# Performance work log

Hardware: AMD Instinct MI355X
Metric: run time of the kernel (lower is better)

## Reference

```python
import jax, jax.numpy as jnp
import numpy as np

B, T, C = 4, 2048, 1024
H_DIM = 1024
N_HEADS = 16
MAX_T = 2048


def setup_inputs() -> dict:
    key = jax.random.key(0)
    ks = jax.random.split(key, 9)
    s = 1.0 / np.sqrt(C)
    return {
        "x": jax.random.normal(ks[0], (B, T, C), dtype=jnp.float32),
        "Wq": jax.random.normal(ks[1], (C, H_DIM), dtype=jnp.float32) * s,
        "bq": jnp.zeros((H_DIM,), dtype=jnp.float32),
        "Wk": jax.random.normal(ks[2], (C, H_DIM), dtype=jnp.float32) * s,
        "bk": jnp.zeros((H_DIM,), dtype=jnp.float32),
        "Wv": jax.random.normal(ks[3], (C, H_DIM), dtype=jnp.float32) * s,
        "bv": jnp.zeros((H_DIM,), dtype=jnp.float32),
        "Wo": jax.random.normal(ks[4], (H_DIM, H_DIM), dtype=jnp.float32) * s,
        "bo": jnp.zeros((H_DIM,), dtype=jnp.float32),
    }


def reference(x, Wq, bq, Wk, bk, Wv, bv, Wo, bo):
    Bx, Tx, Cx = x.shape
    N = N_HEADS
    D = Cx // N
    # QKV projections -> (B, N, T, D)
    q = (x @ Wq + bq).reshape(Bx, Tx, N, D).transpose(0, 2, 1, 3)
    k = (x @ Wk + bk).reshape(Bx, Tx, N, D).transpose(0, 2, 1, 3)
    v = (x @ Wv + bv).reshape(Bx, Tx, N, D).transpose(0, 2, 1, 3)
    # causal scores (B, N, T, T)
    scores = jnp.einsum('bntd,bnfd->bntf', q, k) / jnp.sqrt(jnp.asarray(D, x.dtype))
    causal = jnp.tril(jnp.ones((Tx, Tx), dtype=bool))[None, None]
    scores = jnp.where(causal, scores, -jnp.inf)
    normalized_weights = jax.nn.softmax(scores, axis=-1)
    attention = jnp.einsum('bntf,bnfd->bntd', normalized_weights, v)
    attention = attention.transpose(0, 2, 1, 3).reshape(Bx, Tx, N * D)
    out = attention @ Wo + bo
    return out, normalized_weights
```

## Files before the change

### kernel.cpp

```cpp
#include <hip/hip_runtime.h>

typedef unsigned short UST;
typedef __bf16 v8bf __attribute__((ext_vector_type(8)));
typedef float  v4f  __attribute__((ext_vector_type(4)));

__device__ __forceinline__ UST f2b(float f) {
  union { float f; unsigned u; } x; x.f = f;
  unsigned u = x.u;
  unsigned r = (u + 0x7fffu + ((u >> 16) & 1u)) >> 16;
  return (UST)r;
}

__global__ __launch_bounds__(256) void k_convert(const float* __restrict__ src,
                                                 UST* __restrict__ dst, int n) {
  int i = (blockIdx.x * 256 + threadIdx.x) * 4;
  if (i >= n) return;
  float4 v = *(const float4*)(src + i);
  ushort4 o;
  o.x = f2b(v.x); o.y = f2b(v.y); o.z = f2b(v.z); o.w = f2b(v.w);
  *(ushort4*)(dst + i) = o;
}

__global__ __launch_bounds__(256) void k_transpose(const float* __restrict__ W,
                                                   UST* __restrict__ WT, int R, int C) {
  __shared__ float tile[32][33];
  int tx = threadIdx.x, ty = threadIdx.y;
  int r0 = blockIdx.y * 32, c0 = blockIdx.x * 32;
  for (int i = ty; i < 32; i += 8)
    tile[i][tx] = W[(size_t)(r0 + i) * C + c0 + tx];
  __syncthreads();
  for (int i = ty; i < 32; i += 8)
    WT[(size_t)(c0 + i) * R + r0 + tx] = f2b(tile[tx][i]);
}

__global__ __launch_bounds__(256) void k_gemm_bt(const UST* __restrict__ A,
                                                 const UST* __restrict__ BT,
                                                 const float* __restrict__ bias,
                                                 int M, int N, int K, int mode,
                                                 void* __restrict__ outp) {
  __shared__ UST As[128 * 32];
  __shared__ UST Bs[128 * 32];
  int tid = threadIdx.x;
  int l = tid & 63, w = tid >> 6;
  int g = l >> 4, c16 = l & 15;
  int wm = w >> 1, wn = w & 1;
  int bm = blockIdx.y * 128, bn = blockIdx.x * 128;

  v4f acc[4][4];
  for (int i = 0; i < 4; i++)
    for (int j = 0; j < 4; j++)
      acc[i][j] = (v4f){0.f, 0.f, 0.f, 0.f};

  for (int kb = 0; kb < K; kb += 32) {
    int ch0 = tid, ch1 = tid + 256;
    uint4 a0 = *(const uint4*)(A + (size_t)(bm + (ch0 >> 2)) * K + kb + (ch0 & 3) * 8);
    uint4 a1 = *(const uint4*)(A + (size_t)(bm + (ch1 >> 2)) * K + kb + (ch1 & 3) * 8);
    uint4 b0 = *(const uint4*)(BT + (size_t)(bn + (ch0 >> 2)) * K + kb + (ch0 & 3) * 8);
    uint4 b1 = *(const uint4*)(BT + (size_t)(bn + (ch1 >> 2)) * K + kb + (ch1 & 3) * 8);
    __syncthreads();
    *(uint4*)(As + (size_t)ch0 * 8) = a0;
    *(uint4*)(As + (size_t)ch1 * 8) = a1;
    *(uint4*)(Bs + (size_t)ch0 * 8) = b0;
    *(uint4*)(Bs + (size_t)ch1 * 8) = b1;
    __syncthreads();

    v8bf af[4], bf[4];
    for (int mt = 0; mt < 4; mt++)
      af[mt] = *(const v8bf*)(As + (wm * 64 + mt * 16 + c16) * 32 + g * 8);
    for (int nt = 0; nt < 4; nt++)
      bf[nt] = *(const v8bf*)(Bs + (wn * 64 + nt * 16 + c16) * 32 + g * 8);
    for (int mt = 0; mt < 4; mt++)
      for (int nt = 0; nt < 4; nt++)
        acc[mt][nt] = __builtin_amdgcn_mfma_f32_16x16x32_bf16(af[mt], bf[nt], acc[mt][nt], 0, 0, 0);
  }

  for (int mt = 0; mt < 4; mt++)
    for (int nt = 0; nt < 4; nt++)
      for (int r = 0; r < 4; r++) {
        int row = bm + wm * 64 + mt * 16 + g * 4 + r;
        int col = bn + wn * 64 + nt * 16 + c16;
        float v = acc[mt][nt][r] + bias[col];
        if (mode == 1) {
          int b = row >> 11, t = row & 2047, hn = col >> 6, d = col & 63;
          ((UST*)outp)[((size_t)((b * 16 + hn) * 2048 + t)) * 64 + d] = f2b(v);
        } else if (mode == 2) {
          int b = row >> 11, t = row & 2047, hn = col >> 6, d = col & 63;
          ((UST*)outp)[((size_t)((b * 16 + hn) * 64 + d)) * 2048 + t] = f2b(v);
        } else {
          ((float*)outp)[(size_t)row * N + col] = v;
        }
      }
}

__global__ __launch_bounds__(256) void k_attn(const UST* __restrict__ qh,
                                              const UST* __restrict__ kh,
                                              const UST* __restrict__ vT,
                                              float* __restrict__ Pout,
                                              UST* __restrict__ oh) {
  __shared__ UST Qs[64 * 64];
  __shared__ UST Ks[64 * 64];
  __shared__ UST Pt[4][16 * 32];

  int tid = threadIdx.x;
  int l = tid & 63, w = tid >> 6, g = l >> 4, c16 = l & 15;
  int qt = blockIdx.x, hn = blockIdx.y, b = blockIdx.z;

  const UST* qbase = qh + ((size_t)((b * 16 + hn) * 2048 + qt * 64)) * 64;
  const UST* kbase = kh + ((size_t)((b * 16 + hn) * 2048)) * 64;
  const UST* vbase = vT + ((size_t)((b * 16 + hn) * 64)) * 2048;
  float* pbase = Pout + ((size_t)((b * 16 + hn) * 2048 + qt * 64)) * 2048;

  {
    uint4 t0 = *(const uint4*)(qbase + (size_t)tid * 8);
    uint4 t1 = *(const uint4*)(qbase + (size_t)(tid + 256) * 8);
    *(uint4*)(Qs + (size_t)tid * 8) = t0;
    *(uint4*)(Qs + (size_t)(tid + 256) * 8) = t1;
  }
  __syncthreads();
  v8bf aq0 = *(const v8bf*)(Qs + (w * 16 + c16) * 64 + g * 8);
  v8bf aq1 = *(const v8bf*)(Qs + (w * 16 + c16) * 64 + 32 + g * 8);

  float mrow[4], lrow[4];
  for (int r = 0; r < 4; r++) { mrow[r] = -1e30f; lrow[r] = 0.f; }
  int qrow_base = qt * 64 + w * 16 + g * 4;

  for (int c = 0; c <= qt; c++) {
    uint4 t0 = *(const uint4*)(kbase + (size_t)c * 4096 + (size_t)tid * 8);
    uint4 t1 = *(const uint4*)(kbase + (size_t)c * 4096 + (size_t)(tid + 256) * 8);
    __syncthreads();
    *(uint4*)(Ks + (size_t)tid * 8) = t0;
    *(uint4*)(Ks + (size_t)(tid + 256) * 8) = t1;
    __syncthreads();
    for (int ft = 0; ft < 4; ft++) {
      v8bf b0 = *(const v8bf*)(Ks + (ft * 16 + c16) * 64 + g * 8);
      v8bf b1 = *(const v8bf*)(Ks + (ft * 16 + c16) * 64 + 32 + g * 8);
      v4f s = (v4f){0.f, 0.f, 0.f, 0.f};
      s = __builtin_amdgcn_mfma_f32_16x16x32_bf16(aq0, b0, s, 0, 0, 0);
      s = __builtin_amdgcn_mfma_f32_16x16x32_bf16(aq1, b1, s, 0, 0, 0);
      int f = c * 64 + ft * 16 + c16;
      for (int r = 0; r < 4; r++) {
        bool ok = f <= (qrow_base + r);
        float sv = ok ? s[r] * 0.125f : -1e30f;
        float tm = sv;
        for (int d2 = 1; d2 < 16; d2 <<= 1) tm = fmaxf(tm, __shfl_xor(tm, d2));
        float mn = fmaxf(mrow[r], tm);
        float e = ok ? __expf(sv - mn) : 0.f;
        float ts = e;
        for (int d2 = 1; d2 < 16; d2 <<= 1) ts += __shfl_xor(ts, d2);
        lrow[r] = lrow[r] * __expf(mrow[r] - mn) + ts;
        mrow[r] = mn;
      }
    }
  }

  float rl[4];
  for (int r = 0; r < 4; r++) rl[r] = 1.f / lrow[r];

  v4f accO[4];
  for (int nt = 0; nt < 4; nt++) accO[nt] = (v4f){0.f, 0.f, 0.f, 0.f};

  for (int c = 0; c < 32; c++) {
    bool live = (c <= qt);
    if (live) {
      uint4 t0 = *(const uint4*)(kbase + (size_t)c * 4096 + (size_t)tid * 8);
      uint4 t1 = *(const uint4*)(kbase + (size_t)c * 4096 + (size_t)(tid + 256) * 8);
      __syncthreads();
      *(uint4*)(Ks + (size_t)tid * 8) = t0;
      *(uint4*)(Ks + (size_t)(tid + 256) * 8) = t1;
      __syncthreads();
    }
    for (int fp = 0; fp < 2; fp++) {
      for (int t2 = 0; t2 < 2; t2++) {
        int ft = fp * 2 + t2;
        int f = c * 64 + ft * 16 + c16;
        float pv[4];
        if (live) {
          v8bf b0 = *(const v8bf*)(Ks + (ft * 16 + c16) * 64 + g * 8);
          v8bf b1 = *(const v8bf*)(Ks + (ft * 16 + c16) * 64 + 32 + g * 8);
          v4f s = (v4f){0.f, 0.f, 0.f, 0.f};
          s = __builtin_amdgcn_mfma_f32_16x16x32_bf16(aq0, b0, s, 0, 0, 0);
          s = __builtin_amdgcn_mfma_f32_16x16x32_bf16(aq1, b1, s, 0, 0, 0);
          for (int r = 0; r < 4; r++) {
            bool ok = f <= (qrow_base + r);
            pv[r] = ok ? __expf(s[r] * 0.125f - mrow[r]) * rl[r] : 0.f;
          }
        } else {
          for (int r = 0; r < 4; r++) pv[r] = 0.f;
        }
        for (int r = 0; r < 4; r++) {
          pbase[(size_t)(w * 16 + g * 4 + r) * 2048 + f] = pv[r];
          Pt[w][(g * 4 + r) * 32 + t2 * 16 + c16] = f2b(pv[r]);
        }
      }
      if (live) {
        v8bf pa = *(const v8bf*)(&Pt[w][c16 * 32 + g * 8]);
        for (int nt = 0; nt < 4; nt++) {
          const UST* vp = vbase + (size_t)(nt * 16 + c16) * 2048 + c * 64 + fp * 32 + g * 8;
          v8bf vb = *(const v8bf*)vp;
          accO[nt] = __builtin_amdgcn_mfma_f32_16x16x32_bf16(pa, vb, accO[nt], 0, 0, 0);
        }
      }
    }
  }

  for (int nt = 0; nt < 4; nt++)
    for (int r = 0; r < 4; r++) {
      int qrow = qt * 64 + w * 16 + g * 4 + r;
      int col = hn * 64 + nt * 16 + c16;
      oh[(size_t)(b * 2048 + qrow) * 1024 + col] = f2b(accO[nt][r]);
    }
}

extern "C" void kernel_launch(void* const* d_in, const int* in_sizes, int n_in,
                              void* d_out, int out_size, void* d_ws, size_t ws_size,
                              hipStream_t stream) {
  const float* x  = (const float*)d_in[0];
  const float* Wq = (const float*)d_in[1];
  const float* bq = (const float*)d_in[2];
  const float* Wk = (const float*)d_in[3];
  const float* bk = (const float*)d_in[4];
  const float* Wv = (const float*)d_in[5];
  const float* bv = (const float*)d_in[6];
  const float* Wo = (const float*)d_in[7];
  const float* bo = (const float*)d_in[8];

  float* out  = (float*)d_out;
  float* Pout = out + 8388608;

  UST* xb  = (UST*)d_ws;
  UST* wqT = xb  + 8388608;
  UST* wkT = wqT + 1048576;
  UST* wvT = wkT + 1048576;
  UST* woT = wvT + 1048576;
  UST* qhp = woT + 1048576;
  UST* khp = qhp + 8388608;
  UST* vTp = khp + 8388608;
  UST* ohp = vTp + 8388608;

  k_convert<<<8192, 256, 0, stream>>>(x, xb, 8388608);
  dim3 tb(32, 8), tg(32, 32);
  k_transpose<<<tg, tb, 0, stream>>>(Wq, wqT, 1024, 1024);
  k_transpose<<<tg, tb, 0, stream>>>(Wk, wkT, 1024, 1024);
  k_transpose<<<tg, tb, 0, stream>>>(Wv, wvT, 1024, 1024);
  k_transpose<<<tg, tb, 0, stream>>>(Wo, woT, 1024, 1024);

  dim3 gg(8, 64);
  k_gemm_bt<<<gg, 256, 0, stream>>>(xb, wqT, bq, 8192, 1024, 1024, 1, qhp);
  k_gemm_bt<<<gg, 256, 0, stream>>>(xb, wkT, bk, 8192, 1024, 1024, 1, khp);
  k_gemm_bt<<<gg, 256, 0, stream>>>(xb, wvT, bv, 8192, 1024, 1024, 2, vTp);

  dim3 ag(32, 16, 4);
  k_attn<<<ag, 256, 0, stream>>>(qhp, khp, vTp, Pout, ohp);

  k_gemm_bt<<<gg, 256, 0, stream>>>(ohp, woT, bo, 8192, 1024, 1024, 3, d_out);
}
```

Baseline: 2.298 ms.

## Use direct global-to-LDS loads, exp2 softmax with per-lane stats, vectorized zero fill

Replaces the register-staged global-to-shared copies in the GEMM and attention kernels with global_load_lds direct transfers. The first softmax pass now keeps per-lane running max and sum in exp2 form and does the cross-lane reduction once at the end, removing two shuffle reductions per score tile. The masked upper-triangle region of the probability matrix is written with float4 zero stores in a separate loop instead of scalar stores inside the main loop. Direct LDS loads add a dependence on correct wait handling, and exp2 with a folded scale constant changes rounding slightly.

```diff
diff --git a/kernel.cpp b/kernel.cpp
--- a/kernel.cpp
+++ b/kernel.cpp
@@ -9,6 +9,16 @@
   unsigned u = x.u;
   unsigned r = (u + 0x7fffu + ((u >> 16) & 1u)) >> 16;
   return (UST)r;
+}
+
+__device__ __forceinline__ float fexp2(float x) {
+  return __builtin_amdgcn_exp2f(x);
+}
+
+typedef __attribute__((address_space(3))) unsigned lds_u;
+typedef __attribute__((address_space(1))) const unsigned glb_u;
+__device__ __forceinline__ void gl_lds16(const UST* g, UST* s) {
+  __builtin_amdgcn_global_load_lds((glb_u*)g, (lds_u*)s, 16, 0, 0);
 }
 
 __global__ __launch_bounds__(256) void k_convert(const float* __restrict__ src,
@@ -46,22 +56,23 @@
   int wm = w >> 1, wn = w & 1;
   int bm = blockIdx.y * 128, bn = blockIdx.x * 128;
 
+  int ch0 = tid, ch1 = tid + 256;
+  const UST* a0p = A + (size_t)(bm + (ch0 >> 2)) * K + (ch0 & 3) * 8;
+  const UST* a1p = A + (size_t)(bm + (ch1 >> 2)) * K + (ch1 & 3) * 8;
+  const UST* b0p = BT + (size_t)(bn + (ch0 >> 2)) * K + (ch0 & 3) * 8;
+  const UST* b1p = BT + (size_t)(bn + (ch1 >> 2)) * K + (ch1 & 3) * 8;
+
   v4f acc[4][4];
   for (int i = 0; i < 4; i++)
     for (int j = 0; j < 4; j++)
       acc[i][j] = (v4f){0.f, 0.f, 0.f, 0.f};
 
   for (int kb = 0; kb < K; kb += 32) {
-    int ch0 = tid, ch1 = tid + 256;
-    uint4 a0 = *(const uint4*)(A + (size_t)(bm + (ch0 >> 2)) * K + kb + (ch0 & 3) * 8);
-    uint4 a1 = *(const uint4*)(A + (size_t)(bm + (ch1 >> 2)) * K + kb + (ch1 & 3) * 8);
-    uint4 b0 = *(const uint4*)(BT + (size_t)(bn + (ch0 >> 2)) * K + kb + (ch0 & 3) * 8);
-    uint4 b1 = *(const uint4*)(BT + (size_t)(bn + (ch1 >> 2)) * K + kb + (ch1 & 3) * 8);
-    __syncthreads();
-    *(uint4*)(As + (size_t)ch0 * 8) = a0;
-    *(uint4*)(As + (size_t)ch1 * 8) = a1;
-    *(uint4*)(Bs + (size_t)ch0 * 8) = b0;
-    *(uint4*)(Bs + (size_t)ch1 * 8) = b1;
+    __syncthreads();
+    gl_lds16(a0p + kb, As + (size_t)ch0 * 8);
+    gl_lds16(a1p + kb, As + (size_t)ch1 * 8);
+    gl_lds16(b0p + kb, Bs + (size_t)ch0 * 8);
+    gl_lds16(b1p + kb, Bs + (size_t)ch1 * 8);
     __syncthreads();
 
     v8bf af[4], bf[4];
@@ -110,26 +121,23 @@
   const UST* vbase = vT + ((size_t)((b * 16 + hn) * 64)) * 2048;
   float* pbase = Pout + ((size_t)((b * 16 + hn) * 2048 + qt * 64)) * 2048;
 
-  {
-    uint4 t0 = *(const uint4*)(qbase + (size_t)tid * 8);
-    uint4 t1 = *(const uint4*)(qbase + (size_t)(tid + 256) * 8);
-    *(uint4*)(Qs + (size_t)tid * 8) = t0;
-    *(uint4*)(Qs + (size_t)(tid + 256) * 8) = t1;
-  }
+  const float SC = 0.18033688011f;
+
+  gl_lds16(qbase + (size_t)tid * 8, Qs + (size_t)tid * 8);
+  gl_lds16(qbase + (size_t)(tid + 256) * 8, Qs + (size_t)(tid + 256) * 8);
   __syncthreads();
   v8bf aq0 = *(const v8bf*)(Qs + (w * 16 + c16) * 64 + g * 8);
   v8bf aq1 = *(const v8bf*)(Qs + (w * 16 + c16) * 64 + 32 + g * 8);
 
-  float mrow[4], lrow[4];
-  for (int r = 0; r < 4; r++) { mrow[r] = -1e30f; lrow[r] = 0.f; }
   int qrow_base = qt * 64 + w * 16 + g * 4;
 
+  float mL[4], lL[4];
+  for (int r = 0; r < 4; r++) { mL[r] = -1e30f; lL[r] = 0.f; }
+
   for (int c = 0; c <= qt; c++) {
-    uint4 t0 = *(const uint4*)(kbase + (size_t)c * 4096 + (size_t)tid * 8);
-    uint4 t1 = *(const uint4*)(kbase + (size_t)c * 4096 + (size_t)(tid + 256) * 8);
-    __syncthreads();
-    *(uint4*)(Ks + (size_t)tid * 8) = t0;
-    *(uint4*)(Ks + (size_t)(tid + 256) * 8) = t1;
+    __syncthreads();
+    gl_lds16(kbase + (size_t)c * 4096 + (size_t)tid * 8, Ks + (size_t)tid * 8);
+    gl_lds16(kbase + (size_t)c * 4096 + (size_t)(tid + 256) * 8, Ks + (size_t)(tid + 256) * 8);
     __syncthreads();
     for (int ft = 0; ft < 4; ft++) {
       v8bf b0 = *(const v8bf*)(Ks + (ft * 16 + c16) * 64 + g * 8);
@@ -140,66 +148,63 @@
       int f = c * 64 + ft * 16 + c16;
       for (int r = 0; r < 4; r++) {
         bool ok = f <= (qrow_base + r);
-        float sv = ok ? s[r] * 0.125f : -1e30f;
-        float tm = sv;
-        for (int d2 = 1; d2 < 16; d2 <<= 1) tm = fmaxf(tm, __shfl_xor(tm, d2));
-        float mn = fmaxf(mrow[r], tm);
-        float e = ok ? __expf(sv - mn) : 0.f;
-        float ts = e;
-        for (int d2 = 1; d2 < 16; d2 <<= 1) ts += __shfl_xor(ts, d2);
-        lrow[r] = lrow[r] * __expf(mrow[r] - mn) + ts;
-        mrow[r] = mn;
-      }
-    }
-  }
-
-  float rl[4];
-  for (int r = 0; r < 4; r++) rl[r] = 1.f / lrow[r];
+        float sv = ok ? s[r] * SC : -1e30f;
+        float nm = fmaxf(mL[r], sv);
+        float e2 = fexp2(sv - nm);
+        lL[r] = lL[r] * fexp2(mL[r] - nm) + (ok ? e2 : 0.f);
+        mL[r] = nm;
+      }
+    }
+  }
+
+  float mrow[4], rl[4];
+  for (int r = 0; r < 4; r++) {
+    float tm = mL[r];
+    for (int d = 1; d < 16; d <<= 1) tm = fmaxf(tm, __shfl_xor(tm, d));
+    float t = lL[r] * fexp2(mL[r] - tm);
+    for (int d = 1; d < 16; d <<= 1) t += __shfl_xor(t, d);
+    mrow[r] = tm;
+    rl[r] = 1.f / t;
+  }
 
   v4f accO[4];
   for (int nt = 0; nt < 4; nt++) accO[nt] = (v4f){0.f, 0.f, 0.f, 0.f};
 
-  for (int c = 0; c < 32; c++) {
-    bool live = (c <= qt);
-    if (live) {
-      uint4 t0 = *(const uint4*)(kbase + (size_t)c * 4096 + (size_t)tid * 8);
-      uint4 t1 = *(const uint4*)(kbase + (size_t)c * 4096 + (size_t)(tid + 256) * 8);
-      __syncthreads();
-      *(uint4*)(Ks + (size_t)tid * 8) = t0;
-      *(uint4*)(Ks + (size_t)(tid + 256) * 8) = t1;
-      __syncthreads();
-    }
+  for (int c = 0; c <= qt; c++) {
+    __syncthreads();
+    gl_lds16(kbase + (size_t)c * 4096 + (size_t)tid * 8, Ks + (size_t)tid * 8);
+    gl_lds16(kbase + (size_t)c * 4096 + (size_t)(tid + 256) * 8, Ks + (size_t)(tid + 256) * 8);
+    __syncthreads();
     for (int fp = 0; fp < 2; fp++) {
       for (int t2 = 0; t2 < 2; t2++) {
         int ft = fp * 2 + t2;
+        v8bf b0 = *(const v8bf*)(Ks + (ft * 16 + c16) * 64 + g * 8);
+        v8bf b1 = *(const v8bf*)(Ks + (ft * 16 + c16) * 64 + 32 + g * 8);
+        v4f s = (v4f){0.f, 0.f, 0.f, 0.f};
+        s = __builtin_amdgcn_mfma_f32_16x16x32_bf16(aq0, b0, s, 0, 0, 0);
+        s = __builtin_amdgcn_mfma_f32_16x16x32_bf16(aq1, b1, s, 0, 0, 0);
         int f = c * 64 + ft * 16 + c16;
-        float pv[4];
-        if (live) {
-          v8bf b0 = *(const v8bf*)(Ks + (ft * 16 + c16) * 64 + g * 8);
-          v8bf b1 = *(const v8bf*)(Ks + (ft * 16 + c16) * 64 + 32 + g * 8);
-          v4f s = (v4f){0.f, 0.f, 0.f, 0.f};
-          s = __builtin_amdgcn_mfma_f32_16x16x32_bf16(aq0, b0, s, 0, 0, 0);
-          s = __builtin_amdgcn_mfma_f32_16x16x32_bf16(aq1, b1, s, 0, 0, 0);
-          for (int r = 0; r < 4; r++) {
-            bool ok = f <= (qrow_base + r);
-            pv[r] = ok ? __expf(s[r] * 0.125f - mrow[r]) * rl[r] : 0.f;
-          }
-        } else {
-          for (int r = 0; r < 4; r++) pv[r] = 0.f;
+        for (int r = 0; r < 4; r++) {
+          bool ok = f <= (qrow_base + r);
+          float pv = ok ? fexp2(s[r] * SC - mrow[r]) * rl[r] : 0.f;
+          pbase[(size_t)(w * 16 + g * 4 + r) * 2048 + f] = pv;
+          Pt[w][(g * 4 + r) * 32 + t2 * 16 + c16] = f2b(pv);
         }
-        for (int r = 0; r < 4; r++) {
-          pbase[(size_t)(w * 16 + g * 4 + r) * 2048 + f] = pv[r];
-          Pt[w][(g * 4 + r) * 32 + t2 * 16 + c16] = f2b(pv[r]);
-        }
-      }
-      if (live) {
-        v8bf pa = *(const v8bf*)(&Pt[w][c16 * 32 + g * 8]);
-        for (int nt = 0; nt < 4; nt++) {
-          const UST* vp = vbase + (size_t)(nt * 16 + c16) * 2048 + c * 64 + fp * 32 + g * 8;
-          v8bf vb = *(const v8bf*)vp;
-          accO[nt] = __builtin_amdgcn_mfma_f32_16x16x32_bf16(pa, vb, accO[nt], 0, 0, 0);
-        }
-      }
+      }
+      v8bf pa = *(const v8bf*)(&Pt[w][c16 * 32 + g * 8]);
+      for (int nt = 0; nt < 4; nt++) {
+        const UST* vp = vbase + (size_t)(nt * 16 + c16) * 2048 + c * 64 + fp * 32 + g * 8;
+        v8bf vb = *(const v8bf*)vp;
+        accO[nt] = __builtin_amdgcn_mfma_f32_16x16x32_bf16(pa, vb, accO[nt], 0, 0, 0);
+      }
+    }
+  }
+
+  {
+    float4 z4 = make_float4(0.f, 0.f, 0.f, 0.f);
+    for (int c = qt + 1; c < 32; c++) {
+      float4* zp = (float4*)(pbase + (size_t)(w * 16 + (l >> 2)) * 2048 + c * 64) + (l & 3);
+      zp[0] = z4; zp[4] = z4; zp[8] = z4; zp[12] = z4;
     }
   }
 
```

Result: faster. 2.219 ms (-3.5%).
